# Optimization experiments

Hardware: AMD Instinct MI355X
Metric: run time of the kernel (lower is better)

The kernel has to match this reference:

```python
import jax, jax.numpy as jnp
import numpy as np

B, C, E, H = 8, 2048, 1024, 128


def setup_inputs() -> dict:
    key = jax.random.key(0)
    kx, kq, kk, kv = jax.random.split(key, 4)
    scale = 1.0 / np.sqrt(E)
    return {
        "x": jax.random.normal(kx, (B, C, E), dtype=jnp.float32),
        "Wq": jax.random.normal(kq, (E, H), dtype=jnp.float32) * scale,
        "Wk": jax.random.normal(kk, (E, H), dtype=jnp.float32) * scale,
        "Wv": jax.random.normal(kv, (E, H), dtype=jnp.float32) * scale,
    }


def reference(x, Wq, Wk, Wv):
    # x: (B, C, E); projections -> (B, C, H)
    q = jnp.einsum("bce,eh->bch", x, Wq)
    k = jnp.einsum("bce,eh->bch", x, Wk)
    v = jnp.einsum("bce,eh->bch", x, Wv)
    # NOTE: original scales by sqrt(embed_size), not head_size
    scores = jnp.einsum("bqh,bkh->bqk", q, k) / jnp.sqrt(jnp.asarray(E, x.dtype))
    Cq = x.shape[1]
    causal = jnp.tril(jnp.ones((Cq, Cq), dtype=bool))
    scores = jnp.where(causal, scores, -jnp.inf)
    weights = jax.nn.softmax(scores, axis=-1)  # (B, C, C)
    out = jnp.einsum("bqk,bkh->bqh", weights, v)
    return out
```

## Files before the change

### kernel.cpp

```cpp
#include <hip/hip_runtime.h>
#include <hip/hip_bf16.h>

#define BATCH 8
#define CTX   2048
#define EMB   1024
#define HD    128
#define VSTR  2080

using bf16x8 = __attribute__((ext_vector_type(8))) short;
using fx4    = __attribute__((ext_vector_type(4))) float;

__device__ __forceinline__ ushort f2bf(float f) {
    union { float f; unsigned u; } v; v.f = f;
    unsigned u = v.u;
    u += 0x7fffu + ((u >> 16) & 1u);
    return (ushort)(u >> 16);
}

__device__ __forceinline__ unsigned cvtpk(float a, float b) {
    unsigned r;
    asm("v_cvt_pk_bf16_f32 %0, %1, %2" : "=v"(r) : "v"(a), "v"(b));
    return r;
}

__device__ __forceinline__ float exp2a(float x) {
    float r;
    asm("v_exp_f32 %0, %1" : "=v"(r) : "v"(x));
    return r;
}

__device__ __forceinline__ void gload16(const void* g, void* l) {
    __builtin_amdgcn_global_load_lds(
        (const __attribute__((address_space(1))) unsigned*)g,
        (__attribute__((address_space(3))) unsigned*)l, 16, 0, 0);
}

__global__ void wt_kernel(const float* __restrict__ Wq, const float* __restrict__ Wk,
                          const float* __restrict__ Wv, ushort* __restrict__ Wt) {
    int idx = blockIdx.x * blockDim.x + threadIdx.x;
    int e = idx % EMB;
    int h = (idx / EMB) % HD;
    int w = idx / (EMB * HD);
    const float* W = (w == 0) ? Wq : (w == 1) ? Wk : Wv;
    Wt[idx] = f2bf(W[e * HD + h]);
}

__global__ __launch_bounds__(256) void proj_kernel(
        const float* __restrict__ x, const ushort* __restrict__ Wt,
        ushort* __restrict__ q, ushort* __restrict__ k, ushort* __restrict__ vt) {
    __shared__ __align__(16) float  As[32 * 64];
    __shared__ __align__(16) ushort Bs[192 * 64];

    const int t    = threadIdx.x;
    const int wave = t >> 6;
    const int lane = t & 63;
    const int lo = lane & 15, hi = lane >> 4;
    const int brow = blockIdx.x * 32;
    const int bcol = blockIdx.y * 192;
    const int kph  = (blockIdx.x ^ (blockIdx.y << 3)) & 15;

    const char* Ab = (const char*)As;
    const char* Bb = (const char*)Bs;

    fx4 acc[2][3];
#pragma unroll
    for (int m2 = 0; m2 < 2; m2++)
#pragma unroll
        for (int n = 0; n < 3; n++) acc[m2][n] = fx4{0.f, 0.f, 0.f, 0.f};

    const int arow_s = t >> 4;
    const int acol_s = ((t & 15) ^ (arow_s & 7)) << 2;
    const int brow_s = t >> 3;
    const int bcol_s = ((t & 7) ^ (brow_s & 7)) << 3;
    const int ldsbase = wave * 1024;

    for (int i = 0; i < 16; ++i) {
        const int k0 = ((i + kph) & 15) << 6;
#pragma unroll
        for (int r = 0; r < 2; r++)
            gload16(x + (size_t)(brow + r * 16 + arow_s) * EMB + k0 + acol_s,
                    (char*)As + r * 4096 + ldsbase);
#pragma unroll
        for (int r = 0; r < 6; r++)
            gload16(Wt + (size_t)(bcol + r * 32 + brow_s) * EMB + k0 + bcol_s,
                    (char*)Bs + r * 4096 + ldsbase);
        __syncthreads();

#pragma unroll
        for (int ks = 0; ks < 2; ks++) {
            bf16x8 af[2], bfr[3];
#pragma unroll
            for (int m2 = 0; m2 < 2; m2++) {
                const int rowA = m2 * 16 + lo;
                const unsigned sw = (rowA & 7) << 4;
                const unsigned ub = rowA * 256 + ks * 128 + hi * 32;
                fx4 a0 = *(const fx4*)(Ab + (ub ^ sw));
                fx4 a1 = *(const fx4*)(Ab + ((ub + 16) ^ sw));
                union { unsigned u[4]; bf16x8 v; } pk;
                pk.u[0] = cvtpk(a0[0], a0[1]);
                pk.u[1] = cvtpk(a0[2], a0[3]);
                pk.u[2] = cvtpk(a1[0], a1[1]);
                pk.u[3] = cvtpk(a1[2], a1[3]);
                af[m2] = pk.v;
            }
#pragma unroll
            for (int n = 0; n < 3; n++) {
                const int rowB = wave * 48 + n * 16 + lo;
                const unsigned ub = rowB * 128 + ks * 64 + hi * 16;
                bfr[n] = *(const bf16x8*)(Bb + (ub ^ ((rowB & 7) << 4)));
            }
#pragma unroll
            for (int m2 = 0; m2 < 2; m2++)
#pragma unroll
                for (int n = 0; n < 3; n++)
                    acc[m2][n] = __builtin_amdgcn_mfma_f32_16x16x32_bf16(af[m2], bfr[n], acc[m2][n], 0, 0, 0);
        }
        __syncthreads();
    }

    const float qscale = 0.045084219f;
#pragma unroll
    for (int n = 0; n < 3; n++) {
        const int col = bcol + wave * 48 + n * 16 + lo;
        const int bnn = col >> 7;
        const int cc  = col & 127;
#pragma unroll
        for (int m2 = 0; m2 < 2; m2++) {
#pragma unroll
            for (int j = 0; j < 4; j++) {
                const int r = brow + m2 * 16 + hi * 4 + j;
                if (bnn == 0)      q[(size_t)r * HD + cc] = f2bf(acc[m2][n][j] * qscale);
                else if (bnn == 1) k[(size_t)r * HD + cc] = f2bf(acc[m2][n][j]);
                else {
                    const int bb2 = r >> 11, ccc = r & (CTX - 1);
                    vt[((size_t)bb2 * HD + cc) * VSTR + ccc] = f2bf(acc[m2][n][j]);
                }
            }
        }
    }
}

__global__ __launch_bounds__(256) void attn_kernel(
        const ushort* __restrict__ q, const ushort* __restrict__ k,
        const ushort* __restrict__ vt, float* __restrict__ out) {
    __shared__ __align__(16) char Ks[2][4][8192];
    __shared__ __align__(16) char p_lds[4][1280];

    const int id   = blockIdx.x;
    const int b    = id & 7;
    const int p    = id >> 3;
    const int t    = threadIdx.x;
    const int w    = t >> 6;
    const int lane = t & 63;
    const int lo = lane & 15, hi = lane >> 4;

    const ushort* qb = q  + (size_t)b * CTX * HD;
    const ushort* kb = k  + (size_t)b * CTX * HD;
    const ushort* vb = vt + (size_t)b * HD * VSTR;

    float* oB  = (float*)&Ks[0][0][0];
    float* mlB = (float*)&Ks[0][3][0];

#define KSTAGE(bi, kv0_) do {                                                  \
    _Pragma("unroll")                                                          \
    for (int r = 0; r < 8; ++r) {                                              \
        const int rl  = r * 4 + (lane >> 4);                                   \
        const int key = (rl >> 1) & 7;                                         \
        gload16(kb + (size_t)((kv0_) + w * 32 + rl) * HD + (((lane & 15) ^ key) << 3), \
                Ks[bi][w] + r * 1024);                                         \
    }                                                                          \
} while (0)

    for (int phase = 0; phase < 2; ++phase) {
        const int qt = phase ? p : (127 - p);
        const int q0 = qt * 16;
        const int nkv = qt / 8 + 1;

        bf16x8 qf[4];
#pragma unroll
        for (int ks = 0; ks < 4; ks++)
            qf[ks] = *(const bf16x8*)(qb + (q0 + lo) * HD + ks * 32 + hi * 8);

        fx4 o[8];
#pragma unroll
        for (int h = 0; h < 8; h++) o[h] = fx4{0.f, 0.f, 0.f, 0.f};
        float m[4], l[4];
#pragma unroll
        for (int j = 0; j < 4; j++) { m[j] = 0.f; l[j] = 0.f; }

        KSTAGE(0, 0);

        for (int it = 0; it < nkv; ++it) {
            const int kv0 = it * 128;
            bf16x8 vf[8];
#pragma unroll
            for (int h = 0; h < 8; h++)
                vf[h] = *(const bf16x8*)(vb + (size_t)(h * 16 + lo) * VSTR + kv0 + w * 32 + hi * 8);
            __builtin_amdgcn_sched_barrier(0);
            if (it + 1 < nkv) {
                KSTAGE((it + 1) & 1, kv0 + 128);
                __builtin_amdgcn_sched_barrier(0);
                asm volatile("s_waitcnt vmcnt(16)" ::: "memory");
            } else {
                asm volatile("s_waitcnt vmcnt(8)" ::: "memory");
            }
            __builtin_amdgcn_sched_barrier(0);

            const char* Kb = Ks[it & 1][w];
            fx4 s[2];
            s[0] = fx4{0.f, 0.f, 0.f, 0.f};
            s[1] = fx4{0.f, 0.f, 0.f, 0.f};
            __builtin_amdgcn_s_setprio(1);
#pragma unroll
            for (int n2 = 0; n2 < 2; n2++) {
                const int rl = 2 * lo + n2;
#pragma unroll
                for (int ks = 0; ks < 4; ks++) {
                    bf16x8 kf = *(const bf16x8*)(Kb + rl * 256 + ((ks * 64 + hi * 16) ^ ((lo & 7) << 4)));
                    s[n2] = __builtin_amdgcn_mfma_f32_16x16x32_bf16(qf[ks], kf, s[n2], 0, 0, 0);
                }
            }
            __builtin_amdgcn_s_setprio(0);

            const bool diag = (kv0 + 128 > q0);
            float pmax[4];
            int allok = 1;
#pragma unroll
            for (int j = 0; j < 4; j++) {
                const int r = q0 + hi * 4 + j;
                if (diag) {
                    const int c0 = kv0 + w * 32 + 2 * lo;
                    if (c0 > r)     s[0][j] = -INFINITY;
                    if (c0 + 1 > r) s[1][j] = -INFINITY;
                }
                pmax[j] = fmaxf(s[0][j], s[1][j]);
                allok &= (pmax[j] <= m[j] + 23.0f);
            }
            if (!__all(allok)) {
#pragma unroll
                for (int j = 0; j < 4; j++) {
                    float mx = pmax[j];
                    mx = fmaxf(mx, __shfl_xor(mx, 1));
                    mx = fmaxf(mx, __shfl_xor(mx, 2));
                    mx = fmaxf(mx, __shfl_xor(mx, 4));
                    mx = fmaxf(mx, __shfl_xor(mx, 8));
                    const float mn = fmaxf(m[j], mx);
                    const float f  = exp2a(m[j] - mn);
                    l[j] *= f;
#pragma unroll
                    for (int h = 0; h < 8; h++) o[h][j] *= f;
                    m[j] = mn;
                }
            }
#pragma unroll
            for (int j = 0; j < 4; j++) {
                const float p0 = exp2a(s[0][j] - m[j]);
                const float p1 = exp2a(s[1][j] - m[j]);
                l[j] += p0 + p1;
                *(unsigned*)(p_lds[w] + (hi * 4 + j) * 80 + lo * 4) = cvtpk(p0, p1);
            }
            asm volatile("" ::: "memory");
            bf16x8 pa = *(const bf16x8*)(p_lds[w] + lo * 80 + hi * 16);
            __builtin_amdgcn_s_setprio(1);
#pragma unroll
            for (int h = 0; h < 8; h++)
                o[h] = __builtin_amdgcn_mfma_f32_16x16x32_bf16(pa, vf[h], o[h], 0, 0, 0);
            __builtin_amdgcn_s_setprio(0);
        }

#pragma unroll
        for (int j = 0; j < 4; j++) {
            l[j] += __shfl_xor(l[j], 1);
            l[j] += __shfl_xor(l[j], 2);
            l[j] += __shfl_xor(l[j], 4);
            l[j] += __shfl_xor(l[j], 8);
        }

        __syncthreads();
        if (w > 0) {
#pragma unroll
            for (int j = 0; j < 4; j++) {
                const int row = hi * 4 + j;
                if (lo == 0) { mlB[(w - 1) * 32 + row] = m[j]; mlB[(w - 1) * 32 + 16 + row] = l[j]; }
#pragma unroll
                for (int h = 0; h < 8; h++)
                    oB[(w - 1) * 2048 + row * 128 + h * 16 + lo] = o[h][j];
            }
        }
        __syncthreads();
        if (w == 0) {
            float* ob = out + ((size_t)b * CTX + q0) * HD;
#pragma unroll
            for (int j = 0; j < 4; j++) {
                const int row = hi * 4 + j;
                float mp[3], lp[3];
                float mt = m[j];
#pragma unroll
                for (int pp = 0; pp < 3; pp++) {
                    mp[pp] = mlB[pp * 32 + row];
                    lp[pp] = mlB[pp * 32 + 16 + row];
                    mt = fmaxf(mt, mp[pp]);
                }
                const float f0 = exp2a(m[j] - mt);
                float fp[3];
#pragma unroll
                for (int pp = 0; pp < 3; pp++) fp[pp] = exp2a(mp[pp] - mt);
                const float inv = 1.0f / (l[j] * f0 + lp[0] * fp[0] + lp[1] * fp[1] + lp[2] * fp[2]);
#pragma unroll
                for (int h = 0; h < 8; h++) {
                    float acc = o[h][j] * f0;
#pragma unroll
                    for (int pp = 0; pp < 3; pp++)
                        acc += oB[pp * 2048 + row * 128 + h * 16 + lo] * fp[pp];
                    ob[row * HD + h * 16 + lo] = acc * inv;
                }
            }
        }
        __syncthreads();
        asm volatile("s_waitcnt vmcnt(0)" ::: "memory");
    }
#undef KSTAGE
}

extern "C" void kernel_launch(void* const* d_in, const int* in_sizes, int n_in,
                              void* d_out, int out_size, void* d_ws, size_t ws_size,
                              hipStream_t stream) {
    const float* x  = (const float*)d_in[0];
    const float* Wq = (const float*)d_in[1];
    const float* Wk = (const float*)d_in[2];
    const float* Wv = (const float*)d_in[3];

    ushort* Wt = (ushort*)d_ws;
    ushort* qw = (ushort*)((char*)d_ws + 786432);
    ushort* kw = qw + (size_t)BATCH * CTX * HD;
    ushort* vw = kw + (size_t)BATCH * CTX * HD;

    wt_kernel<<<(3 * HD * EMB) / 256, 256, 0, stream>>>(Wq, Wk, Wv, Wt);
    proj_kernel<<<dim3(512, 2), 256, 0, stream>>>(x, Wt, qw, kw, vw);
    attn_kernel<<<512, 256, 0, stream>>>(qw, kw, vw, (float*)d_out);
}
```

Before: 84.83 us.

## Split attention KV tile across eight waves instead of four

The attention kernel now launches 512 threads per block, so eight waves each own 16 keys of the 128-key tile instead of four waves owning 32. Each wave does half the QK MFMAs and writes a narrower P tile. The PV MFMA still runs at full K=32 width, with half the lanes feeding zeros, and the final cross-wave merge now combines seven partial results instead of three. This aims for more latency hiding and parallelism per query tile, at the cost of wasted PV MFMA work, a larger reduction, and more registers per block, which may reduce occupancy.

```diff
diff --git a/kernel.cpp b/kernel.cpp
--- a/kernel.cpp
+++ b/kernel.cpp
@@ -140,11 +140,11 @@
     }
 }
 
-__global__ __launch_bounds__(256) void attn_kernel(
+__global__ void attn_kernel(
         const ushort* __restrict__ q, const ushort* __restrict__ k,
         const ushort* __restrict__ vt, float* __restrict__ out) {
-    __shared__ __align__(16) char Ks[2][4][8192];
-    __shared__ __align__(16) char p_lds[4][1280];
+    __shared__ __align__(16) char Ks[2][8][4096];
+    __shared__ __align__(16) char p_lds[8][768];
 
     const int id   = blockIdx.x;
     const int b    = id & 7;
@@ -159,14 +159,14 @@
     const ushort* vb = vt + (size_t)b * HD * VSTR;
 
     float* oB  = (float*)&Ks[0][0][0];
-    float* mlB = (float*)&Ks[0][3][0];
+    float* mlB = (float*)((char*)&Ks[0][0][0] + 57344);
 
 #define KSTAGE(bi, kv0_) do {                                                  \
     _Pragma("unroll")                                                          \
-    for (int r = 0; r < 8; ++r) {                                              \
+    for (int r = 0; r < 4; ++r) {                                              \
         const int rl  = r * 4 + (lane >> 4);                                   \
-        const int key = (rl >> 1) & 7;                                         \
-        gload16(kb + (size_t)((kv0_) + w * 32 + rl) * HD + (((lane & 15) ^ key) << 3), \
+        const int key = rl & 7;                                                \
+        gload16(kb + (size_t)((kv0_) + w * 16 + rl) * HD + (((lane & 15) ^ key) << 3), \
                 Ks[bi][w] + r * 1024);                                         \
     }                                                                          \
 } while (0)
@@ -179,7 +179,7 @@
         bf16x8 qf[4];
 #pragma unroll
         for (int ks = 0; ks < 4; ks++)
-            qf[ks] = *(const bf16x8*)(qb + (q0 + lo) * HD + ks * 32 + hi * 8);
+            qf[ks] = *(const bf16x8*)(qb + (size_t)(q0 + lo) * HD + ks * 32 + hi * 8);
 
         fx4 o[8];
 #pragma unroll
@@ -195,51 +195,41 @@
             bf16x8 vf[8];
 #pragma unroll
             for (int h = 0; h < 8; h++)
-                vf[h] = *(const bf16x8*)(vb + (size_t)(h * 16 + lo) * VSTR + kv0 + w * 32 + hi * 8);
+                vf[h] = *(const bf16x8*)(vb + (size_t)(h * 16 + lo) * VSTR
+                                         + kv0 + w * 16 + (hi & 1) * 8);
             __builtin_amdgcn_sched_barrier(0);
             if (it + 1 < nkv) {
                 KSTAGE((it + 1) & 1, kv0 + 128);
                 __builtin_amdgcn_sched_barrier(0);
-                asm volatile("s_waitcnt vmcnt(16)" ::: "memory");
+                asm volatile("s_waitcnt vmcnt(12)" ::: "memory");
             } else {
                 asm volatile("s_waitcnt vmcnt(8)" ::: "memory");
             }
             __builtin_amdgcn_sched_barrier(0);
 
             const char* Kb = Ks[it & 1][w];
-            fx4 s[2];
-            s[0] = fx4{0.f, 0.f, 0.f, 0.f};
-            s[1] = fx4{0.f, 0.f, 0.f, 0.f};
+            fx4 s = fx4{0.f, 0.f, 0.f, 0.f};
             __builtin_amdgcn_s_setprio(1);
 #pragma unroll
-            for (int n2 = 0; n2 < 2; n2++) {
-                const int rl = 2 * lo + n2;
-#pragma unroll
-                for (int ks = 0; ks < 4; ks++) {
-                    bf16x8 kf = *(const bf16x8*)(Kb + rl * 256 + ((ks * 64 + hi * 16) ^ ((lo & 7) << 4)));
-                    s[n2] = __builtin_amdgcn_mfma_f32_16x16x32_bf16(qf[ks], kf, s[n2], 0, 0, 0);
-                }
+            for (int ks = 0; ks < 4; ks++) {
+                bf16x8 kf = *(const bf16x8*)(Kb + lo * 256 + ((ks * 64 + hi * 16) ^ ((lo & 7) << 4)));
+                s = __builtin_amdgcn_mfma_f32_16x16x32_bf16(qf[ks], kf, s, 0, 0, 0);
             }
             __builtin_amdgcn_s_setprio(0);
 
             const bool diag = (kv0 + 128 > q0);
-            float pmax[4];
+            const int  c    = kv0 + w * 16 + lo;
             int allok = 1;
 #pragma unroll
             for (int j = 0; j < 4; j++) {
                 const int r = q0 + hi * 4 + j;
-                if (diag) {
-                    const int c0 = kv0 + w * 32 + 2 * lo;
-                    if (c0 > r)     s[0][j] = -INFINITY;
-                    if (c0 + 1 > r) s[1][j] = -INFINITY;
-                }
-                pmax[j] = fmaxf(s[0][j], s[1][j]);
-                allok &= (pmax[j] <= m[j] + 23.0f);
+                if (diag && c > r) s[j] = -INFINITY;
+                allok &= (s[j] <= m[j] + 23.0f);
             }
             if (!__all(allok)) {
 #pragma unroll
                 for (int j = 0; j < 4; j++) {
-                    float mx = pmax[j];
+                    float mx = s[j];
                     mx = fmaxf(mx, __shfl_xor(mx, 1));
                     mx = fmaxf(mx, __shfl_xor(mx, 2));
                     mx = fmaxf(mx, __shfl_xor(mx, 4));
@@ -254,13 +244,13 @@
             }
 #pragma unroll
             for (int j = 0; j < 4; j++) {
-                const float p0 = exp2a(s[0][j] - m[j]);
-                const float p1 = exp2a(s[1][j] - m[j]);
-                l[j] += p0 + p1;
-                *(unsigned*)(p_lds[w] + (hi * 4 + j) * 80 + lo * 4) = cvtpk(p0, p1);
+                const float pv = exp2a(s[j] - m[j]);
+                l[j] += pv;
+                *(ushort*)(p_lds[w] + (hi * 4 + j) * 40 + lo * 2) = f2bf(pv);
             }
             asm volatile("" ::: "memory");
-            bf16x8 pa = *(const bf16x8*)(p_lds[w] + lo * 80 + hi * 16);
+            bf16x8 pa = bf16x8{0, 0, 0, 0, 0, 0, 0, 0};
+            if (hi < 2) pa = *(const bf16x8*)(p_lds[w] + lo * 40 + hi * 16);
             __builtin_amdgcn_s_setprio(1);
 #pragma unroll
             for (int h = 0; h < 8; h++)
@@ -293,24 +283,23 @@
 #pragma unroll
             for (int j = 0; j < 4; j++) {
                 const int row = hi * 4 + j;
-                float mp[3], lp[3];
                 float mt = m[j];
 #pragma unroll
-                for (int pp = 0; pp < 3; pp++) {
-                    mp[pp] = mlB[pp * 32 + row];
-                    lp[pp] = mlB[pp * 32 + 16 + row];
-                    mt = fmaxf(mt, mp[pp]);
+                for (int pp = 0; pp < 7; pp++) mt = fmaxf(mt, mlB[pp * 32 + row]);
+                const float f0 = exp2a(m[j] - mt);
+                float lsum = l[j] * f0;
+                float fp[7];
+#pragma unroll
+                for (int pp = 0; pp < 7; pp++) {
+                    fp[pp] = exp2a(mlB[pp * 32 + row] - mt);
+                    lsum += mlB[pp * 32 + 16 + row] * fp[pp];
                 }
-                const float f0 = exp2a(m[j] - mt);
-                float fp[3];
-#pragma unroll
-                for (int pp = 0; pp < 3; pp++) fp[pp] = exp2a(mp[pp] - mt);
-                const float inv = 1.0f / (l[j] * f0 + lp[0] * fp[0] + lp[1] * fp[1] + lp[2] * fp[2]);
+                const float inv = 1.0f / lsum;
 #pragma unroll
                 for (int h = 0; h < 8; h++) {
                     float acc = o[h][j] * f0;
 #pragma unroll
-                    for (int pp = 0; pp < 3; pp++)
+                    for (int pp = 0; pp < 7; pp++)
                         acc += oB[pp * 2048 + row * 128 + h * 16 + lo] * fp[pp];
                     ob[row * HD + h * 16 + lo] = acc * inv;
                 }
@@ -337,5 +326,5 @@
 
     wt_kernel<<<(3 * HD * EMB) / 256, 256, 0, stream>>>(Wq, Wk, Wv, Wt);
     proj_kernel<<<dim3(512, 2), 256, 0, stream>>>(x, Wt, qw, kw, vw);
-    attn_kernel<<<512, 256, 0, stream>>>(qw, kw, vw, (float*)d_out);
-}
+    attn_kernel<<<512, 512, 0, stream>>>(qw, kw, vw, (float*)d_out);
+}
```

Measured after the change: 214.9 us. 153% more time.

## Software-pipeline QK^T one KV tile ahead of softmax and PV in attention loop

Applied to the files above, without the earlier changes.

Restructures the attention inner loop so the QK^T MFMA for the next KV tile runs after the softmax of the current tile and before its PV MFMAs. The K prefetch moves two tiles ahead into the freed double buffer, and a prologue computes the first score tile. The aim is to overlap the exp/softmax VALU work with matrix-core work and hide K load latency. It costs extra score registers and manual vmcnt bookkeeping, and with only two K buffers the prefetch of tile it+2 reuses buffer it&1, which could race with loads if the waitcnt counting is off.

```diff
diff --git a/kernel.cpp b/kernel.cpp
--- a/kernel.cpp
+++ b/kernel.cpp
@@ -171,6 +171,23 @@
     }                                                                          \
 } while (0)
 
+#define QKCOMP(Kb_, sd) do {                                                   \
+    sd[0] = fx4{0.f, 0.f, 0.f, 0.f};                                           \
+    sd[1] = fx4{0.f, 0.f, 0.f, 0.f};                                           \
+    __builtin_amdgcn_s_setprio(1);                                             \
+    _Pragma("unroll")                                                          \
+    for (int n2 = 0; n2 < 2; n2++) {                                           \
+        const int rl = 2 * lo + n2;                                            \
+        _Pragma("unroll")                                                      \
+        for (int ks = 0; ks < 4; ks++) {                                       \
+            bf16x8 kf = *(const bf16x8*)((Kb_) + rl * 256 +                    \
+                         ((ks * 64 + hi * 16) ^ ((lo & 7) << 4)));             \
+            sd[n2] = __builtin_amdgcn_mfma_f32_16x16x32_bf16(qf[ks], kf, sd[n2], 0, 0, 0); \
+        }                                                                      \
+    }                                                                          \
+    __builtin_amdgcn_s_setprio(0);                                             \
+} while (0)
+
     for (int phase = 0; phase < 2; ++phase) {
         const int qt = phase ? p : (127 - p);
         const int q0 = qt * 16;
@@ -179,7 +196,7 @@
         bf16x8 qf[4];
 #pragma unroll
         for (int ks = 0; ks < 4; ks++)
-            qf[ks] = *(const bf16x8*)(qb + (q0 + lo) * HD + ks * 32 + hi * 8);
+            qf[ks] = *(const bf16x8*)(qb + (size_t)(q0 + lo) * HD + ks * 32 + hi * 8);
 
         fx4 o[8];
 #pragma unroll
@@ -188,7 +205,12 @@
 #pragma unroll
         for (int j = 0; j < 4; j++) { m[j] = 0.f; l[j] = 0.f; }
 
+        fx4 sA[2], sB[2];
         KSTAGE(0, 0);
+        asm volatile("s_waitcnt vmcnt(0)" ::: "memory");
+        __builtin_amdgcn_sched_barrier(0);
+        QKCOMP(Ks[0][w], sA);
+        if (nkv > 1) KSTAGE(1, 128);
 
         for (int it = 0; it < nkv; ++it) {
             const int kv0 = it * 128;
@@ -197,30 +219,10 @@
             for (int h = 0; h < 8; h++)
                 vf[h] = *(const bf16x8*)(vb + (size_t)(h * 16 + lo) * VSTR + kv0 + w * 32 + hi * 8);
             __builtin_amdgcn_sched_barrier(0);
-            if (it + 1 < nkv) {
-                KSTAGE((it + 1) & 1, kv0 + 128);
+            if (it + 2 < nkv) {
+                KSTAGE(it & 1, kv0 + 256);
                 __builtin_amdgcn_sched_barrier(0);
-                asm volatile("s_waitcnt vmcnt(16)" ::: "memory");
-            } else {
-                asm volatile("s_waitcnt vmcnt(8)" ::: "memory");
-            }
-            __builtin_amdgcn_sched_barrier(0);
-
-            const char* Kb = Ks[it & 1][w];
-            fx4 s[2];
-            s[0] = fx4{0.f, 0.f, 0.f, 0.f};
-            s[1] = fx4{0.f, 0.f, 0.f, 0.f};
-            __builtin_amdgcn_s_setprio(1);
-#pragma unroll
-            for (int n2 = 0; n2 < 2; n2++) {
-                const int rl = 2 * lo + n2;
-#pragma unroll
-                for (int ks = 0; ks < 4; ks++) {
-                    bf16x8 kf = *(const bf16x8*)(Kb + rl * 256 + ((ks * 64 + hi * 16) ^ ((lo & 7) << 4)));
-                    s[n2] = __builtin_amdgcn_mfma_f32_16x16x32_bf16(qf[ks], kf, s[n2], 0, 0, 0);
-                }
-            }
-            __builtin_amdgcn_s_setprio(0);
+            }
 
             const bool diag = (kv0 + 128 > q0);
             float pmax[4];
@@ -230,10 +232,10 @@
                 const int r = q0 + hi * 4 + j;
                 if (diag) {
                     const int c0 = kv0 + w * 32 + 2 * lo;
-                    if (c0 > r)     s[0][j] = -INFINITY;
-                    if (c0 + 1 > r) s[1][j] = -INFINITY;
-                }
-                pmax[j] = fmaxf(s[0][j], s[1][j]);
+                    if (c0 > r)     sA[0][j] = -INFINITY;
+                    if (c0 + 1 > r) sA[1][j] = -INFINITY;
+                }
+                pmax[j] = fmaxf(sA[0][j], sA[1][j]);
                 allok &= (pmax[j] <= m[j] + 23.0f);
             }
             if (!__all(allok)) {
@@ -254,18 +256,28 @@
             }
 #pragma unroll
             for (int j = 0; j < 4; j++) {
-                const float p0 = exp2a(s[0][j] - m[j]);
-                const float p1 = exp2a(s[1][j] - m[j]);
+                const float p0 = exp2a(sA[0][j] - m[j]);
+                const float p1 = exp2a(sA[1][j] - m[j]);
                 l[j] += p0 + p1;
                 *(unsigned*)(p_lds[w] + (hi * 4 + j) * 80 + lo * 4) = cvtpk(p0, p1);
             }
             asm volatile("" ::: "memory");
+            if (it + 1 < nkv) {
+                if (it + 2 < nkv)
+                    asm volatile("s_waitcnt vmcnt(16)" ::: "memory");
+                else
+                    asm volatile("s_waitcnt vmcnt(8)" ::: "memory");
+                __builtin_amdgcn_sched_barrier(0);
+                QKCOMP(Ks[(it + 1) & 1][w], sB);
+            }
             bf16x8 pa = *(const bf16x8*)(p_lds[w] + lo * 80 + hi * 16);
             __builtin_amdgcn_s_setprio(1);
 #pragma unroll
             for (int h = 0; h < 8; h++)
                 o[h] = __builtin_amdgcn_mfma_f32_16x16x32_bf16(pa, vf[h], o[h], 0, 0, 0);
             __builtin_amdgcn_s_setprio(0);
+            sA[0] = sB[0];
+            sA[1] = sB[1];
         }
 
 #pragma unroll
@@ -320,6 +332,7 @@
         asm volatile("s_waitcnt vmcnt(0)" ::: "memory");
     }
 #undef KSTAGE
+#undef QKCOMP
 }
 
 extern "C" void kernel_launch(void* const* d_in, const int* in_sizes, int n_in,
```

After: 99.11 us. 1.17x slower.

## Split attention KV loop across 8 waves with single-buffered K tiles

Applied to the files above, without the earlier changes.

The attention kernel now launches 512 threads (8 waves) per block instead of 4, so each iteration covers a 256-key tile and the number of KV iterations per query tile is halved. The double-buffered K staging in LDS becomes a single buffer, and the next tile's load is issued after the QK MFMAs finish reading LDS. The final merge combines partial softmax states from 7 waves instead of 3. The aim is more parallelism per query tile, shorter serial KV loops and an LDS footprint that allows more resident blocks. The cost is less overlap between the K prefetch and compute, plus a larger cross-wave reduction.

```diff
diff --git a/kernel.cpp b/kernel.cpp
--- a/kernel.cpp
+++ b/kernel.cpp
@@ -140,11 +140,11 @@
     }
 }
 
-__global__ __launch_bounds__(256) void attn_kernel(
+__global__ __launch_bounds__(512, 4) void attn_kernel(
         const ushort* __restrict__ q, const ushort* __restrict__ k,
         const ushort* __restrict__ vt, float* __restrict__ out) {
-    __shared__ __align__(16) char Ks[2][4][8192];
-    __shared__ __align__(16) char p_lds[4][1280];
+    __shared__ __align__(16) char Ks[8][8192];
+    __shared__ __align__(16) char p_lds[8][1280];
 
     const int id   = blockIdx.x;
     const int b    = id & 7;
@@ -158,28 +158,28 @@
     const ushort* kb = k  + (size_t)b * CTX * HD;
     const ushort* vb = vt + (size_t)b * HD * VSTR;
 
-    float* oB  = (float*)&Ks[0][0][0];
-    float* mlB = (float*)&Ks[0][3][0];
-
-#define KSTAGE(bi, kv0_) do {                                                  \
+    float* oB  = (float*)&Ks[0][0];
+    float* mlB = (float*)((char*)&Ks[0][0] + 57344);
+
+#define KSTAGE(kv0_) do {                                                      \
     _Pragma("unroll")                                                          \
     for (int r = 0; r < 8; ++r) {                                              \
         const int rl  = r * 4 + (lane >> 4);                                   \
         const int key = (rl >> 1) & 7;                                         \
         gload16(kb + (size_t)((kv0_) + w * 32 + rl) * HD + (((lane & 15) ^ key) << 3), \
-                Ks[bi][w] + r * 1024);                                         \
+                Ks[w] + r * 1024);                                             \
     }                                                                          \
 } while (0)
 
     for (int phase = 0; phase < 2; ++phase) {
         const int qt = phase ? p : (127 - p);
         const int q0 = qt * 16;
-        const int nkv = qt / 8 + 1;
+        const int nkv = qt / 16 + 1;
 
         bf16x8 qf[4];
 #pragma unroll
         for (int ks = 0; ks < 4; ks++)
-            qf[ks] = *(const bf16x8*)(qb + (q0 + lo) * HD + ks * 32 + hi * 8);
+            qf[ks] = *(const bf16x8*)(qb + (size_t)(q0 + lo) * HD + ks * 32 + hi * 8);
 
         fx4 o[8];
 #pragma unroll
@@ -188,25 +188,18 @@
 #pragma unroll
         for (int j = 0; j < 4; j++) { m[j] = 0.f; l[j] = 0.f; }
 
-        KSTAGE(0, 0);
+        KSTAGE(0);
 
         for (int it = 0; it < nkv; ++it) {
-            const int kv0 = it * 128;
+            const int kv0 = it * 256;
             bf16x8 vf[8];
 #pragma unroll
             for (int h = 0; h < 8; h++)
                 vf[h] = *(const bf16x8*)(vb + (size_t)(h * 16 + lo) * VSTR + kv0 + w * 32 + hi * 8);
             __builtin_amdgcn_sched_barrier(0);
-            if (it + 1 < nkv) {
-                KSTAGE((it + 1) & 1, kv0 + 128);
-                __builtin_amdgcn_sched_barrier(0);
-                asm volatile("s_waitcnt vmcnt(16)" ::: "memory");
-            } else {
-                asm volatile("s_waitcnt vmcnt(8)" ::: "memory");
-            }
+            asm volatile("s_waitcnt vmcnt(8)" ::: "memory");
             __builtin_amdgcn_sched_barrier(0);
 
-            const char* Kb = Ks[it & 1][w];
             fx4 s[2];
             s[0] = fx4{0.f, 0.f, 0.f, 0.f};
             s[1] = fx4{0.f, 0.f, 0.f, 0.f};
@@ -216,13 +209,19 @@
                 const int rl = 2 * lo + n2;
 #pragma unroll
                 for (int ks = 0; ks < 4; ks++) {
-                    bf16x8 kf = *(const bf16x8*)(Kb + rl * 256 + ((ks * 64 + hi * 16) ^ ((lo & 7) << 4)));
+                    bf16x8 kf = *(const bf16x8*)(Ks[w] + rl * 256 + ((ks * 64 + hi * 16) ^ ((lo & 7) << 4)));
                     s[n2] = __builtin_amdgcn_mfma_f32_16x16x32_bf16(qf[ks], kf, s[n2], 0, 0, 0);
                 }
             }
             __builtin_amdgcn_s_setprio(0);
-
-            const bool diag = (kv0 + 128 > q0);
+            if (it + 1 < nkv) {
+                asm volatile("s_waitcnt lgkmcnt(0)" ::: "memory");
+                __builtin_amdgcn_sched_barrier(0);
+                KSTAGE(kv0 + 256);
+                __builtin_amdgcn_sched_barrier(0);
+            }
+
+            const bool diag = (kv0 + 256 > q0);
             float pmax[4];
             int allok = 1;
 #pragma unroll
@@ -293,24 +292,23 @@
 #pragma unroll
             for (int j = 0; j < 4; j++) {
                 const int row = hi * 4 + j;
-                float mp[3], lp[3];
                 float mt = m[j];
 #pragma unroll
-                for (int pp = 0; pp < 3; pp++) {
-                    mp[pp] = mlB[pp * 32 + row];
-                    lp[pp] = mlB[pp * 32 + 16 + row];
-                    mt = fmaxf(mt, mp[pp]);
-                }
+                for (int pp = 0; pp < 7; pp++) mt = fmaxf(mt, mlB[pp * 32 + row]);
                 const float f0 = exp2a(m[j] - mt);
-                float fp[3];
-#pragma unroll
-                for (int pp = 0; pp < 3; pp++) fp[pp] = exp2a(mp[pp] - mt);
-                const float inv = 1.0f / (l[j] * f0 + lp[0] * fp[0] + lp[1] * fp[1] + lp[2] * fp[2]);
+                float lsum = l[j] * f0;
+                float fp[7];
+#pragma unroll
+                for (int pp = 0; pp < 7; pp++) {
+                    fp[pp] = exp2a(mlB[pp * 32 + row] - mt);
+                    lsum += mlB[pp * 32 + 16 + row] * fp[pp];
+                }
+                const float inv = 1.0f / lsum;
 #pragma unroll
                 for (int h = 0; h < 8; h++) {
                     float acc = o[h][j] * f0;
 #pragma unroll
-                    for (int pp = 0; pp < 3; pp++)
+                    for (int pp = 0; pp < 7; pp++)
                         acc += oB[pp * 2048 + row * 128 + h * 16 + lo] * fp[pp];
                     ob[row * HD + h * 16 + lo] = acc * inv;
                 }
@@ -337,5 +335,5 @@
 
     wt_kernel<<<(3 * HD * EMB) / 256, 256, 0, stream>>>(Wq, Wk, Wv, Wt);
     proj_kernel<<<dim3(512, 2), 256, 0, stream>>>(x, Wt, qw, kw, vw);
-    attn_kernel<<<512, 256, 0, stream>>>(qw, kw, vw, (float*)d_out);
-}
+    attn_kernel<<<512, 512, 0, stream>>>(qw, kw, vw, (float*)d_out);
+}
```

Result: slower. 105.0 us (+23.8%).
